# Kernel optimization log

Measured on AMD Instinct MI355X. Metric: run time of the kernel, lower is better.

The kernel has to match this reference:

```python
import jax, jax.numpy as jnp
import numpy as np

B, R, H, IN, L = 8, 128, 256, 512, 3
NH, DH = 4, H // 4  # attention heads


def _layernorm(x, g, b, eps=1e-5):
    mu = jnp.mean(x, axis=-1, keepdims=True)
    var = jnp.mean(jnp.square(x - mu), axis=-1, keepdims=True)
    return (x - mu) * jax.lax.rsqrt(var + eps) * g + b


def setup_inputs() -> dict:
    key = jax.random.key(0)
    ks = iter(jax.random.split(key, 40))
    s = 0.02
    d = {}
    d['x'] = jax.random.normal(next(ks), (B, IN), jnp.float32)
    d['We'] = jax.random.normal(next(ks), (IN, H), jnp.float32) * s
    d['be'] = jnp.zeros((H,), jnp.float32)
    # per-graph-layer params, stacked along leading L axis
    d['msg_W1'] = jax.random.normal(next(ks), (L, 2 * H, H), jnp.float32) * s
    d['msg_b1'] = jnp.zeros((L, H), jnp.float32)
    d['msg_W2'] = jax.random.normal(next(ks), (L, H, H), jnp.float32) * s
    d['msg_b2'] = jnp.zeros((L, H), jnp.float32)
    d['upd_W1'] = jax.random.normal(next(ks), (L, 2 * H, H), jnp.float32) * s
    d['upd_b1'] = jnp.zeros((L, H), jnp.float32)
    d['upd_W2'] = jax.random.normal(next(ks), (L, H, H), jnp.float32) * s
    d['upd_b2'] = jnp.zeros((L, H), jnp.float32)
    d['ln_g'] = jnp.ones((L, H), jnp.float32)
    d['ln_b'] = jnp.zeros((L, H), jnp.float32)
    d['rule_adj'] = jax.random.normal(next(ks), (R, R), jnp.float32)
    # multihead attention (4 heads)
    d['Wq'] = jax.random.normal(next(ks), (H, H), jnp.float32) * s
    d['bq'] = jnp.zeros((H,), jnp.float32)
    d['Wk'] = jax.random.normal(next(ks), (H, H), jnp.float32) * s
    d['bk'] = jnp.zeros((H,), jnp.float32)
    d['Wv'] = jax.random.normal(next(ks), (H, H), jnp.float32) * s
    d['bv'] = jnp.zeros((H,), jnp.float32)
    d['Wo'] = jax.random.normal(next(ks), (H, H), jnp.float32) * s
    d['bo'] = jnp.zeros((H,), jnp.float32)
    # readout MLP -> num_rules logits
    d['ro_W1'] = jax.random.normal(next(ks), (H, H), jnp.float32) * s
    d['ro_b1'] = jnp.zeros((H,), jnp.float32)
    d['ro_W2'] = jax.random.normal(next(ks), (H, R), jnp.float32) * s
    d['ro_b2'] = jnp.zeros((R,), jnp.float32)
    return d


def reference(x, We, be, msg_W1, msg_b1, msg_W2, msg_b2,
              upd_W1, upd_b1, upd_W2, upd_b2, ln_g, ln_b, rule_adj,
              Wq, bq, Wk, bk, Wv, bv, Wo, bo,
              ro_W1, ro_b1, ro_W2, ro_b2):
    # node encoder, broadcast to all rule-graph nodes: [B,R,H]
    h0 = x @ We + be
    h = jnp.broadcast_to(h0[:, None, :], (B, R, H))
    # rule adjacency with self-edges excluded (loop used i != j)
    A = jax.nn.sigmoid(rule_adj) * (1.0 - jnp.eye(R, dtype=rule_adj.dtype))  # [R,R]
    for l in range(L):
        # message_net(cat(h_i, h_j)) = relu(h_i@W1a + h_j@W1b + b1)@W2 + b2
        W1a, W1b = msg_W1[l][:H], msg_W1[l][H:]
        a = h @ W1a   # [B,R,H] (receiver i part)
        bb = h @ W1b  # [B,R,H] (sender j part)
        pre = jax.nn.relu(a[:, :, None, :] + bb[:, None, :, :] + msg_b1[l])  # [B,R,R,H]
        m = pre @ msg_W2[l] + msg_b2[l]  # [B,R,R,H] message from j to i
        agg = jnp.einsum('bijh,ij->bih', m, A)  # weighted sum over senders j
        # update_net(cat(h, agg))
        Wu1a, Wu1b = upd_W1[l][:H], upd_W1[l][H:]
        u = jax.nn.relu(h @ Wu1a + agg @ Wu1b + upd_b1[l]) @ upd_W2[l] + upd_b2[l]
        h = _layernorm(h + u, ln_g[l], ln_b[l])
    # multihead self-attention over nodes
    q = (h @ Wq + bq).reshape(B, R, NH, DH)
    k = (h @ Wk + bk).reshape(B, R, NH, DH)
    v = (h @ Wv + bv).reshape(B, R, NH, DH)
    logits = jnp.einsum('bqhd,bkhd->bhqk', q, k) / jnp.sqrt(jnp.float32(DH))
    attn = jax.nn.softmax(logits, axis=-1)
    pooled = jnp.einsum('bhqk,bkhd->bqhd', attn, v).reshape(B, R, H) @ Wo + bo
    g = jnp.mean(pooled, axis=1)  # [B,H]
    rule_logits = jax.nn.relu(g @ ro_W1 + ro_b1) @ ro_W2 + ro_b2
    rule_probabilities = jax.nn.softmax(rule_logits, axis=-1)  # [B,R]
    return rule_probabilities
```

## Files before the change

kernel.cpp:

```cpp
#include <hip/hip_runtime.h>
#include <math.h>

constexpr int NB  = 8;
constexpr int NR  = 128;
constexpr int HID = 256;
constexpr int NIN = 512;
constexpr int DHD = 64;
constexpr size_t SZ = (size_t)NB * NR * HID;

struct KP {
    const float *x, *We, *be, *msg_W1, *msg_b1, *msg_W2, *msg_b2;
    const float *upd_W1, *upd_b1, *upd_W2, *upd_b2, *ln_g, *ln_b, *rule_adj;
    const float *Wq, *bq, *Wk, *bk, *Wv, *bv, *Wo, *bo, *ro_W1, *ro_b1, *ro_W2, *ro_b2;
    float* out;
    float *hu0, *hu1, *hu2;
    float *bufA, *bufBB, *bufP1, *bufU1;
    float *W2u, *mb2u, *Aw, *rsum;
    float *mW1s;
    float *h0g, *c0g, *c1g;
    float *gacc;
    float *sts;
    float *scratch;
};

__device__ __forceinline__ void gemm_core(
    float (&As)[16][68], float (&Bs)[16][64], int m0, int n0,
    const float* __restrict__ A, const float* __restrict__ B,
    float (&acc)[4][4])
{
    int tid = threadIdx.x;
    int ty = tid >> 4, tx = tid & 15;
    int arow = tid >> 2, acol = (tid & 3) << 2;
    int brow = tid >> 4, bcol = (tid & 15) << 2;
    int m = m0 + arow;

    auto loadA = [&](int k0) -> float4 {
        return *(const float4*)&A[(size_t)m * HID + k0 + acol];
    };

    float4 av = loadA(0);
    float4 bv = *(const float4*)&B[(size_t)brow * HID + n0 + bcol];

    for (int k0 = 0; k0 < HID; k0 += 16) {
        As[acol + 0][arow] = av.x;
        As[acol + 1][arow] = av.y;
        As[acol + 2][arow] = av.z;
        As[acol + 3][arow] = av.w;
        *(float4*)&Bs[brow][bcol] = bv;
        __syncthreads();
        if (k0 + 16 < HID) {
            av = loadA(k0 + 16);
            bv = *(const float4*)&B[(size_t)(k0 + 16 + brow) * HID + n0 + bcol];
        }
#pragma unroll
        for (int kk = 0; kk < 16; ++kk) {
            float4 af = *(const float4*)&As[kk][ty << 2];
            float4 bf = *(const float4*)&Bs[kk][tx << 2];
            float a_[4] = {af.x, af.y, af.z, af.w};
            float b_[4] = {bf.x, bf.y, bf.z, bf.w};
#pragma unroll
            for (int i = 0; i < 4; ++i)
#pragma unroll
                for (int j = 0; j < 4; ++j) acc[i][j] += a_[i] * b_[j];
        }
        __syncthreads();
    }
}

__device__ __forceinline__ void gemv256w(
    const float* xs, const float* __restrict__ W,
    const float* __restrict__ bias, int relu, float* ys, float* red)
{
    int tid = threadIdx.x;
    int w = tid >> 6, l = tid & 63;
    float4 acc = {0.f, 0.f, 0.f, 0.f};
    const float* Wp = W + (size_t)(w * 64) * HID + l * 4;
    const float* xp = xs + w * 64;
#pragma unroll 16
    for (int kk = 0; kk < 64; ++kk) {
        float xv = xp[kk];
        float4 wv = *(const float4*)(Wp + (size_t)kk * HID);
        acc.x += xv * wv.x; acc.y += xv * wv.y;
        acc.z += xv * wv.z; acc.w += xv * wv.w;
    }
    *(float4*)&red[w * 256 + l * 4] = acc;
    __syncthreads();
    float v = red[tid] + red[256 + tid] + red[512 + tid] + red[768 + tid];
    if (bias) v += bias[tid];
    if (relu) v = fmaxf(v, 0.0f);
    ys[tid] = v;
    __syncthreads();
}

__global__ __launch_bounds__(256) void setup0_kernel(KP P) {
    __shared__ union {
        struct { float As[16][68]; float Bs[16][64]; } g;
        struct { float xs[NIN]; float part[8][32]; } e;
    } L;
    int blk = blockIdx.x;
    int t = threadIdx.x;

    if (blk < 32) {
        int rr = blk * 4 + (t >> 6);
        int l = t & 63;
        float s_loc = 0.f;
#pragma unroll
        for (int rep = 0; rep < 2; ++rep) {
            int j = l + rep * 64;
            float xv = P.rule_adj[rr * NR + j];
            float sg = 1.0f / (1.0f + expf(-xv));
            if (j == rr) sg = 0.0f;
            P.Aw[rr * NR + j] = sg;
            s_loc += sg;
        }
#pragma unroll
        for (int off = 32; off; off >>= 1) s_loc += __shfl_xor(s_loc, off);
        if (l == 0) P.rsum[rr] = s_loc;
    } else if (blk < 80) {
        int idx = blk - 32, l2 = idx >> 4, t16 = idx & 15;
        int m0 = (t16 >> 2) * 64, n0 = (t16 & 3) * 64;
        float acc[4][4] = {};
        gemm_core(L.g.As, L.g.Bs, m0, n0,
                  P.msg_W2 + (size_t)l2 * HID * HID,
                  P.upd_W1 + (size_t)l2 * 2 * HID * HID + (size_t)HID * HID,
                  acc);
        int ty = t >> 4, tx = t & 15;
        float* C = P.W2u + (size_t)l2 * HID * HID;
#pragma unroll
        for (int i = 0; i < 4; ++i) {
            int m = m0 + (ty << 2) + i, n = n0 + (tx << 2);
            float4 o = {acc[i][0], acc[i][1], acc[i][2], acc[i][3]};
            *(float4*)&C[(size_t)m * HID + n] = o;
        }
    } else if (blk < 83) {
        int l2 = blk - 80;
        const float* b2v = P.msg_b2 + l2 * HID;
        const float* Bm = P.upd_W1 + (size_t)l2 * 2 * HID * HID + (size_t)HID * HID;
        float acc = 0.f;
#pragma unroll 4
        for (int k = 0; k < HID; ++k) acc += b2v[k] * Bm[(size_t)k * HID + t];
        P.mb2u[l2 * HID + t] = acc;
    } else if (blk < 147) {
        int idx = blk - 83;
        int b = idx >> 3, s = idx & 7;
        L.e.xs[t]       = P.x[b * NIN + t];
        L.e.xs[256 + t] = P.x[b * NIN + 256 + t];
        __syncthreads();
        int c = t & 31, seg = t >> 5;
        int col = s * 32 + c;
        const float* Wp = P.We + (size_t)(seg * 64) * HID + col;
        const float* xp = L.e.xs + seg * 64;
        float acc = 0.f;
#pragma unroll 16
        for (int k = 0; k < 64; ++k) acc += xp[k] * Wp[(size_t)k * HID];
        L.e.part[seg][c] = acc;
        __syncthreads();
        if (t < 32) {
            float v = 0.f;
#pragma unroll
            for (int sg = 0; sg < 8; ++sg) v += L.e.part[sg][t];
            int cc = s * 32 + t;
            P.h0g[b * HID + cc] = v + P.be[cc];
        }
    } else if (blk < 163) {
        int base = (blk - 147) * 4096;
        for (int i = t; i < 4096; i += 256) {
            int o = base + i;
            P.mW1s[o] = P.msg_W1[o] + P.msg_W1[65536 + o];
        }
    } else {
        int pfid = blk - 163, npf = 256 - 163;
        const float* arr[11] = {P.We, P.msg_W1, P.msg_W2, P.upd_W1, P.upd_W2,
                                P.Wq, P.Wk, P.Wv, P.Wo, P.ro_W1, P.ro_W2};
        const int n4[11] = {32768, 98304, 49152, 98304, 49152,
                            16384, 16384, 16384, 16384, 16384, 8192};
        float s = 0.f;
        for (int a = 0; a < 11; ++a) {
            const float4* p4 = (const float4*)arr[a];
            for (int i = pfid * 256 + t; i < n4[a]; i += npf * 256) {
                float4 v = p4[i];
                s += v.x + v.y + v.z + v.w;
            }
        }
        if (s == 1.0e37f) P.scratch[pfid] = s;
    }
}

__global__ __launch_bounds__(256) void headc_kernel(KP P) {
    __shared__ float h0s[HID];
    __shared__ float p0s[HID];
    __shared__ float part[8][32];
    int blk = blockIdx.x;
    int z = blk >> 6, bs = blk & 63;
    int b = bs >> 3, s = bs & 7;
    int t = threadIdx.x;
    h0s[t] = P.h0g[b * HID + t];
    __syncthreads();
    const float* Wslice;
    const float* xs;
    if (z == 0) {
        Wslice = P.upd_W1;
        xs = h0s;
    } else {
        float accp = 0.f;
#pragma unroll 8
        for (int k = 0; k < HID; ++k)
            accp += h0s[k] * P.mW1s[(size_t)k * HID + t];
        p0s[t] = fmaxf(accp + P.msg_b1[t], 0.0f);
        __syncthreads();
        Wslice = P.W2u;
        xs = p0s;
    }
    int c = t & 31, seg = t >> 5;
    int col = s * 32 + c;
    const float* Wp = Wslice + (size_t)(seg * 32) * HID + col;
    const float* xp = xs + seg * 32;
    float acc = 0.f;
#pragma unroll 8
    for (int k = 0; k < 32; ++k) acc += xp[k] * Wp[(size_t)k * HID];
    part[seg][c] = acc;
    __syncthreads();
    if (t < 32) {
        float v = 0.f;
#pragma unroll
        for (int sg = 0; sg < 8; ++sg) v += part[sg][t];
        int cc = s * 32 + t;
        if (z == 0) P.c0g[b * HID + cc] = v;
        else        P.c1g[b * HID + cc] = v + P.mb2u[cc];
    }
}

__device__ __forceinline__ void rows4_matmul(
    const float (&rows)[4][HID], const float* __restrict__ W, int n, float o[4])
{
    o[0] = o[1] = o[2] = o[3] = 0.f;
#pragma unroll 4
    for (int k0 = 0; k0 < HID; k0 += 4) {
        float w0 = W[(size_t)(k0 + 0) * HID + n];
        float w1 = W[(size_t)(k0 + 1) * HID + n];
        float w2 = W[(size_t)(k0 + 2) * HID + n];
        float w3 = W[(size_t)(k0 + 3) * HID + n];
#pragma unroll
        for (int ii = 0; ii < 4; ++ii) {
            float4 rv = *(const float4*)&rows[ii][k0];
            o[ii] += rv.x * w0 + rv.y * w1 + rv.z * w2 + rv.w * w3;
        }
    }
}

__device__ __forceinline__ void row_stats4(
    float (&sred)[4][4][2], const float v[4], float* sts, float* stq, int m0)
{
    int w = threadIdx.x >> 6, l = threadIdx.x & 63;
    float s[4], q[4];
#pragma unroll
    for (int ii = 0; ii < 4; ++ii) { s[ii] = v[ii]; q[ii] = v[ii] * v[ii]; }
#pragma unroll
    for (int off = 32; off; off >>= 1) {
#pragma unroll
        for (int ii = 0; ii < 4; ++ii) {
            s[ii] += __shfl_xor(s[ii], off);
            q[ii] += __shfl_xor(q[ii], off);
        }
    }
    if (l == 0) {
#pragma unroll
        for (int ii = 0; ii < 4; ++ii) { sred[w][ii][0] = s[ii]; sred[w][ii][1] = q[ii]; }
    }
    __syncthreads();
    if (threadIdx.x < 8) {
        int row = threadIdx.x >> 1, isq = threadIdx.x & 1;
        float tot = sred[0][row][isq] + sred[1][row][isq] +
                    sred[2][row][isq] + sred[3][row][isq];
        (isq ? stq : sts)[m0 + row] = tot;
    }
}

__global__ __launch_bounds__(256) void layer0r_kernel(KP P) {
    __shared__ float u1s[4][HID];
    __shared__ float sred[4][4][2];
    int blk = blockIdx.x;
    int m0 = blk * 4;
    int b = m0 >> 7, i0 = m0 & 127;
    int t = threadIdx.x;

    float c0v = P.c0g[b * HID + t];
    float c1v = P.c1g[b * HID + t];
    float ubv = P.upd_b1[t];
#pragma unroll
    for (int ii = 0; ii < 4; ++ii)
        u1s[ii][t] = fmaxf(c0v + P.rsum[i0 + ii] * c1v + ubv, 0.0f);
    __syncthreads();

    float u[4];
    rows4_matmul(u1s, P.upd_W2, t, u);

    float h0v = P.h0g[b * HID + t] + P.upd_b2[t];
    float v[4];
#pragma unroll
    for (int ii = 0; ii < 4; ++ii) {
        v[ii] = u[ii] + h0v;
        P.hu0[(size_t)(m0 + ii) * HID + t] = v[ii];
    }
    __syncthreads();
    row_stats4(sred, v, P.sts, P.sts + 1024, m0);
}

__global__ __launch_bounds__(256) void gemm3_kernel(
    const float* __restrict__ A, const float* __restrict__ ssum, const float* __restrict__ ssq,
    const float* __restrict__ lng, const float* __restrict__ lnb,
    const float* __restrict__ B0, const float* __restrict__ B1, const float* __restrict__ B2,
    const float* __restrict__ bias0, const float* __restrict__ bias1, const float* __restrict__ bias2,
    float* __restrict__ C0, float* __restrict__ C1, float* __restrict__ C2)
{
    __shared__ float As[32][36];
    __shared__ float Bs[32][64];
    int blk = blockIdx.x;
    int z = blk >> 7, tile = blk & 127;
    const float* B    = (z == 0) ? B0 : (z == 1) ? B1 : B2;
    const float* bias = (z == 0) ? bias0 : (z == 1) ? bias1 : bias2;
    float* C          = (z == 0) ? C0 : (z == 1) ? C1 : C2;
    int m0 = (tile >> 2) * 32, n0 = (tile & 3) * 64;

    int tid = threadIdx.x;
    int ar = tid >> 3;
    int acol = (tid & 7) << 2;
    int brow = tid >> 4;
    int bcol = (tid & 15) << 2;
    int m = m0 + ar;

    bool ln = (ssum != nullptr);
    float mu = 0.f, inv = 1.f;
    if (ln) {
        float s = ssum[m], q = ssq[m];
        mu = s * (1.0f / HID);
        inv = rsqrtf(q * (1.0f / HID) - mu * mu + 1e-5f);
    }
    auto loadA = [&](int k0) -> float4 {
        int kx = k0 + acol;
        float4 v = *(const float4*)&A[(size_t)m * HID + kx];
        if (ln) {
            float4 g = *(const float4*)(lng + kx);
            float4 b = *(const float4*)(lnb + kx);
            v.x = (v.x - mu) * inv * g.x + b.x;
            v.y = (v.y - mu) * inv * g.y + b.y;
            v.z = (v.z - mu) * inv * g.z + b.z;
            v.w = (v.w - mu) * inv * g.w + b.w;
        }
        return v;
    };

    float acc[2][4] = {};
    float4 av  = loadA(0);
    float4 bv0 = *(const float4*)&B[(size_t)brow * HID + n0 + bcol];
    float4 bv1 = *(const float4*)&B[(size_t)(16 + brow) * HID + n0 + bcol];

    int ty = tid >> 4, tx = tid & 15;
    int r0 = ty << 1;

    for (int k0 = 0; k0 < HID; k0 += 32) {
        As[acol + 0][ar] = av.x;
        As[acol + 1][ar] = av.y;
        As[acol + 2][ar] = av.z;
        As[acol + 3][ar] = av.w;
        *(float4*)&Bs[brow][bcol]      = bv0;
        *(float4*)&Bs[brow + 16][bcol] = bv1;
        __syncthreads();
        if (k0 + 32 < HID) {
            av  = loadA(k0 + 32);
            bv0 = *(const float4*)&B[(size_t)(k0 + 32 + brow) * HID + n0 + bcol];
            bv1 = *(const float4*)&B[(size_t)(k0 + 48 + brow) * HID + n0 + bcol];
        }
#pragma unroll
        for (int kk = 0; kk < 32; ++kk) {
            float a0 = As[kk][r0];
            float a1 = As[kk][r0 + 1];
            float4 bf = *(const float4*)&Bs[kk][tx << 2];
            acc[0][0] += a0 * bf.x; acc[0][1] += a0 * bf.y;
            acc[0][2] += a0 * bf.z; acc[0][3] += a0 * bf.w;
            acc[1][0] += a1 * bf.x; acc[1][1] += a1 * bf.y;
            acc[1][2] += a1 * bf.z; acc[1][3] += a1 * bf.w;
        }
        __syncthreads();
    }

#pragma unroll
    for (int i = 0; i < 2; ++i) {
        int mm = m0 + r0 + i, n = n0 + (tx << 2);
        float4 o = {acc[i][0], acc[i][1], acc[i][2], acc[i][3]};
        if (bias) {
            float4 bb = *(const float4*)&bias[n];
            o.x += bb.x; o.y += bb.y; o.z += bb.z; o.w += bb.w;
        }
        *(float4*)&C[(size_t)mm * HID + n] = o;
    }
}

__global__ __launch_bounds__(256) void agg_u1r_kernel(
    const float* __restrict__ a, const float* __restrict__ bbv,
    const float* __restrict__ mb1, const float* __restrict__ Aw,
    const float* __restrict__ P1, const float* __restrict__ W2u,
    const float* __restrict__ mb2u, const float* __restrict__ rsum,
    const float* __restrict__ ub1,
    const float* __restrict__ uW2, const float* __restrict__ ub2,
    const float* __restrict__ huprev, const float* __restrict__ sP, const float* __restrict__ qP,
    const float* __restrict__ lngp, const float* __restrict__ lnbp,
    float* __restrict__ hunew, float* __restrict__ sN, float* __restrict__ qN,
    float* __restrict__ gzero)
{
    __shared__ float ap[4][HID];
    __shared__ float u1s[4][HID];
    __shared__ float sred[4][4][2];
    int blk = blockIdx.x;
    int b  = blk >> 5;
    int i0 = (blk & 31) * 4;
    int m0 = b * NR + i0;
    int t  = threadIdx.x;

    if (gzero && blk == 0) {
#pragma unroll
        for (int i = 0; i < 8; ++i) gzero[i * 256 + t] = 0.f;
    }

    float bias = mb1[t];
    float ai[4], acc[4] = {0.f, 0.f, 0.f, 0.f};
#pragma unroll
    for (int ii = 0; ii < 4; ++ii)
        ai[ii] = a[(size_t)(m0 + ii) * HID + t] + bias;
    const float* bbb = &bbv[(size_t)b * NR * HID + t];
#pragma unroll 4
    for (int j = 0; j < NR; ++j) {
        float bj = bbb[(size_t)j * HID];
#pragma unroll
        for (int ii = 0; ii < 4; ++ii) {
            float pre = fmaxf(ai[ii] + bj, 0.0f);
            acc[ii] += Aw[(i0 + ii) * NR + j] * pre;
        }
    }
#pragma unroll
    for (int ii = 0; ii < 4; ++ii) ap[ii][t] = acc[ii];
    __syncthreads();

    float w2[4];
    rows4_matmul(ap, W2u, t, w2);
    float mbv = mb2u[t], ubv = ub1[t];
#pragma unroll
    for (int ii = 0; ii < 4; ++ii) {
        float vv = w2[ii] + P1[(size_t)(m0 + ii) * HID + t] + rsum[i0 + ii] * mbv + ubv;
        u1s[ii][t] = fmaxf(vv, 0.0f);
    }
    __syncthreads();

    float u[4];
    rows4_matmul(u1s, uW2, t, u);

    float gv = lngp[t], btv = lnbp[t], ub2v = ub2[t];
    float v[4];
#pragma unroll
    for (int ii = 0; ii < 4; ++ii) {
        int m = m0 + ii;
        float sp = sP[m], qp = qP[m];
        float mup = sp * (1.0f / HID);
        float invp = rsqrtf(qp * (1.0f / HID) - mup * mup + 1e-5f);
        float hp = huprev[(size_t)m * HID + t];
        v[ii] = (hp - mup) * invp * gv + btv + u[ii] + ub2v;
        hunew[(size_t)m * HID + t] = v[ii];
    }
    __syncthreads();
    row_stats4(sred, v, sN, qN, m0);
}

__global__ __launch_bounds__(256) void attention_kernel(
    const float* __restrict__ q, const float* __restrict__ k,
    const float* __restrict__ v, float* __restrict__ gacc)
{
    __shared__ struct { float KhT[64][128]; float S[16][128]; float qs[16][64]; } L;
    int blk = blockIdx.x;
    int bh = blk >> 3, ig = blk & 7;
    int b = bh >> 2, hd = bh & 3;
    int i0 = ig * 16;
    int t = threadIdx.x;
    const float* qg = q + ((size_t)b * NR) * HID + hd * DHD;
    const float* kg = k + ((size_t)b * NR) * HID + hd * DHD;
    const float* vg = v + ((size_t)b * NR) * HID + hd * DHD;

    {
        int j = t >> 1, half = t & 1;
        const float* krow = kg + (size_t)j * HID + half * 32;
#pragma unroll
        for (int c = 0; c < 32; c += 4) {
            float4 kv = *(const float4*)(krow + c);
            L.KhT[half * 32 + c + 0][j] = kv.x;
            L.KhT[half * 32 + c + 1][j] = kv.y;
            L.KhT[half * 32 + c + 2][j] = kv.z;
            L.KhT[half * 32 + c + 3][j] = kv.w;
        }
    }
    {
        int ii = t >> 4, d0 = (t & 15) * 4;
        *(float4*)&L.qs[ii][d0] = *(const float4*)(qg + (size_t)(i0 + ii) * HID + d0);
    }
    __syncthreads();
    {
        int j = t & 127, ii2 = t >> 7;
        float acc[8] = {0.f,0.f,0.f,0.f,0.f,0.f,0.f,0.f};
#pragma unroll 4
        for (int d = 0; d < 64; ++d) {
            float kv = L.KhT[d][j];
#pragma unroll
            for (int ii = 0; ii < 8; ++ii) acc[ii] += L.qs[ii2 * 8 + ii][d] * kv;
        }
#pragma unroll
        for (int ii = 0; ii < 8; ++ii) L.S[ii2 * 8 + ii][j] = acc[ii] * 0.125f;
    }
    __syncthreads();
    {
        int w = t >> 6, l = t & 63;
#pragma unroll
        for (int r = w * 4; r < w * 4 + 4; ++r) {
            float e0 = L.S[r][l], e1 = L.S[r][l + 64];
            float mx = fmaxf(e0, e1);
#pragma unroll
            for (int off = 32; off; off >>= 1) mx = fmaxf(mx, __shfl_xor(mx, off));
            e0 = expf(e0 - mx); e1 = expf(e1 - mx);
            float sm = e0 + e1;
#pragma unroll
            for (int off = 32; off; off >>= 1) sm += __shfl_xor(sm, off);
            float inv = 1.0f / sm;
            L.S[r][l] = e0 * inv; L.S[r][l + 64] = e1 * inv;
        }
    }
    __syncthreads();
    {
        int d = t & 63, ir = t >> 6;
        float accv[4] = {0.f, 0.f, 0.f, 0.f};
        const float* vp = vg + d;
#pragma unroll 8
        for (int j = 0; j < NR; ++j) {
            float vv = vp[(size_t)j * HID];
#pragma unroll
            for (int p = 0; p < 4; ++p) accv[p] += L.S[p * 4 + ir][j] * vv;
        }
        float s = accv[0] + accv[1] + accv[2] + accv[3];
        atomicAdd(&gacc[b * HID + hd * DHD + d], s);
    }
}

__global__ __launch_bounds__(256) void tailf_kernel(KP P) {
    __shared__ float v0[HID], v1[HID], v2[HID];
    __shared__ float red[1024];
    int b = blockIdx.x;
    int t = threadIdx.x;
    int w = t >> 6, l = t & 63;

    v0[t] = P.gacc[b * HID + t] * (1.0f / NR);
    __syncthreads();
    gemv256w(v0, P.Wo, P.bo, 0, v1, red);
    gemv256w(v1, P.ro_W1, P.ro_b1, 1, v2, red);

    {
        float2 acc = {0.f, 0.f};
        const float* Wp = P.ro_W2 + (size_t)(w * 64) * NR + l * 2;
        const float* xp = v2 + w * 64;
#pragma unroll 8
        for (int kk = 0; kk < 64; ++kk) {
            float xv = xp[kk];
            float2 wv = *(const float2*)(Wp + (size_t)kk * NR);
            acc.x += xv * wv.x; acc.y += xv * wv.y;
        }
        *(float2*)&red[w * 128 + l * 2] = acc;
        __syncthreads();
    }
    float logit = -1e30f;
    if (t < NR) logit = red[t] + red[128 + t] + red[256 + t] + red[384 + t] + P.ro_b2[t];
    __syncthreads();
    float m = logit;
#pragma unroll
    for (int off = 32; off; off >>= 1) m = fmaxf(m, __shfl_xor(m, off));
    if (l == 0) red[w] = m;
    __syncthreads();
    m = fmaxf(red[0], red[1]);
    float e = (t < NR) ? expf(logit - m) : 0.0f;
    float ssum = e;
#pragma unroll
    for (int off = 32; off; off >>= 1) ssum += __shfl_xor(ssum, off);
    if (l == 0) red[4 + w] = ssum;
    __syncthreads();
    float tot = red[4] + red[5];
    if (t < NR) P.out[b * NR + t] = e / tot;
}

extern "C" void kernel_launch(void* const* d_in, const int* in_sizes, int n_in,
                              void* d_out, int out_size, void* d_ws, size_t ws_size,
                              hipStream_t stream)
{
    KP P;
    P.x        = (const float*)d_in[0];
    P.We       = (const float*)d_in[1];
    P.be       = (const float*)d_in[2];
    P.msg_W1   = (const float*)d_in[3];
    P.msg_b1   = (const float*)d_in[4];
    P.msg_W2   = (const float*)d_in[5];
    P.msg_b2   = (const float*)d_in[6];
    P.upd_W1   = (const float*)d_in[7];
    P.upd_b1   = (const float*)d_in[8];
    P.upd_W2   = (const float*)d_in[9];
    P.upd_b2   = (const float*)d_in[10];
    P.ln_g     = (const float*)d_in[11];
    P.ln_b     = (const float*)d_in[12];
    P.rule_adj = (const float*)d_in[13];
    P.Wq       = (const float*)d_in[14];
    P.bq       = (const float*)d_in[15];
    P.Wk       = (const float*)d_in[16];
    P.bk       = (const float*)d_in[17];
    P.Wv       = (const float*)d_in[18];
    P.bv       = (const float*)d_in[19];
    P.Wo       = (const float*)d_in[20];
    P.bo       = (const float*)d_in[21];
    P.ro_W1    = (const float*)d_in[22];
    P.ro_b1    = (const float*)d_in[23];
    P.ro_W2    = (const float*)d_in[24];
    P.ro_b2    = (const float*)d_in[25];
    P.out      = (float*)d_out;

    float* b0 = (float*)d_ws;
    P.hu0    = b0;  b0 += SZ;
    P.hu1    = b0;  b0 += SZ;
    P.hu2    = b0;  b0 += SZ;
    P.bufA   = b0;  b0 += SZ;
    P.bufBB  = b0;  b0 += SZ;
    P.bufP1  = b0;  b0 += SZ;
    P.bufU1  = b0;  b0 += SZ;
    P.W2u    = b0;  b0 += 3 * HID * HID;
    P.mb2u   = b0;  b0 += 3 * HID;
    P.mW1s   = b0;  b0 += HID * HID;
    P.Aw     = b0;  b0 += NR * NR;
    P.rsum   = b0;  b0 += NR;
    P.h0g    = b0;  b0 += NB * HID;
    P.c0g    = b0;  b0 += NB * HID;
    P.c1g    = b0;  b0 += NB * HID;
    P.gacc   = b0;  b0 += NB * HID;
    P.sts    = b0;  b0 += 3 * 2048;
    P.scratch= b0;  b0 += 256;

    const float* hu[3] = {P.hu0, P.hu1, P.hu2};

    setup0_kernel<<<dim3(256), 256, 0, stream>>>(P);

    headc_kernel<<<dim3(128), 256, 0, stream>>>(P);

    layer0r_kernel<<<dim3(256), 256, 0, stream>>>(P);

    for (int l = 1; l < 3; ++l) {
        const float* mW1 = P.msg_W1 + (size_t)l * 2 * HID * HID;
        const float* sP  = P.sts + (l - 1) * 2048;
        const float* qP  = sP + 1024;
        const float* lgp = P.ln_g + (size_t)(l - 1) * HID;
        const float* lbp = P.ln_b + (size_t)(l - 1) * HID;

        gemm3_kernel<<<dim3(384), 256, 0, stream>>>(
            hu[l - 1], sP, qP, lgp, lbp,
            mW1, mW1 + (size_t)HID * HID, P.upd_W1 + (size_t)l * 2 * HID * HID,
            nullptr, nullptr, nullptr,
            P.bufA, P.bufBB, P.bufP1);

        agg_u1r_kernel<<<dim3(256), 256, 0, stream>>>(
            P.bufA, P.bufBB, P.msg_b1 + (size_t)l * HID, P.Aw,
            P.bufP1, P.W2u + (size_t)l * HID * HID,
            P.mb2u + l * HID, P.rsum, P.upd_b1 + (size_t)l * HID,
            P.upd_W2 + (size_t)l * HID * HID, P.upd_b2 + (size_t)l * HID,
            hu[l - 1], sP, qP, lgp, lbp,
            (float*)hu[l], P.sts + l * 2048, P.sts + l * 2048 + 1024,
            (l == 2) ? P.gacc : nullptr);
    }

    gemm3_kernel<<<dim3(384), 256, 0, stream>>>(
        hu[2], P.sts + 2 * 2048, P.sts + 2 * 2048 + 1024,
        P.ln_g + 2 * HID, P.ln_b + 2 * HID,
        P.Wq, P.Wk, P.Wv, P.bq, P.bk, P.bv,
        P.bufA, P.bufBB, P.bufU1);

    attention_kernel<<<dim3(256), 256, 0, stream>>>(P.bufA, P.bufBB, P.bufU1, P.gacc);

    tailf_kernel<<<dim3(8), 256, 0, stream>>>(P);
}
```

Measured before the change: 274.5 us.

## Fuse layernorm and next-layer projections into aggregation kernels, drop GEMM launches

Removes the separate gemm3 launches. Each row-block kernel now computes its own full layernorm and immediately runs the next layer's three projections (msg W1a/W1b, upd W1a, or Q/K/V) on those 4 normalized rows, using per-thread rows4_matmul. Buffers are double-buffered (aB/aA) so the fused kernel can write next-layer inputs while reading the current ones. It also stages adjacency rows in shared memory. The cost is that the projections switch from tiled shared-memory GEMMs to 4-row matvecs, which re-read the weight matrices once per 4-row block and so generate more global/L2 weight traffic.

After: 293.0 us. +6.8%, slower.

```diff
diff --git a/kernel.cpp b/kernel.cpp
--- a/kernel.cpp
+++ b/kernel.cpp
@@ -13,13 +13,13 @@
     const float *upd_W1, *upd_b1, *upd_W2, *upd_b2, *ln_g, *ln_b, *rule_adj;
     const float *Wq, *bq, *Wk, *bk, *Wv, *bv, *Wo, *bo, *ro_W1, *ro_b1, *ro_W2, *ro_b2;
     float* out;
-    float *hu0, *hu1, *hu2;
-    float *bufA, *bufBB, *bufP1, *bufU1;
+    float *N0, *N1, *N2;
+    float *aB, *bbB, *p1B;
+    float *aA, *bbA, *p1A;
     float *W2u, *mb2u, *Aw, *rsum;
     float *mW1s;
     float *h0g, *c0g, *c1g;
     float *gacc;
-    float *sts;
     float *scratch;
 };
 
@@ -34,11 +34,7 @@
     int brow = tid >> 4, bcol = (tid & 15) << 2;
     int m = m0 + arow;
 
-    auto loadA = [&](int k0) -> float4 {
-        return *(const float4*)&A[(size_t)m * HID + k0 + acol];
-    };
-
-    float4 av = loadA(0);
+    float4 av = *(const float4*)&A[(size_t)m * HID + acol];
     float4 bv = *(const float4*)&B[(size_t)brow * HID + n0 + bcol];
 
     for (int k0 = 0; k0 < HID; k0 += 16) {
@@ -49,7 +45,7 @@
         *(float4*)&Bs[brow][bcol] = bv;
         __syncthreads();
         if (k0 + 16 < HID) {
-            av = loadA(k0 + 16);
+            av = *(const float4*)&A[(size_t)m * HID + k0 + 16 + acol];
             bv = *(const float4*)&B[(size_t)(k0 + 16 + brow) * HID + n0 + bcol];
         }
 #pragma unroll
@@ -89,6 +85,55 @@
     if (bias) v += bias[tid];
     if (relu) v = fmaxf(v, 0.0f);
     ys[tid] = v;
+    __syncthreads();
+}
+
+__device__ __forceinline__ void rows4_matmul(
+    const float (&rows)[4][HID], const float* __restrict__ W, int n, float o[4])
+{
+    o[0] = o[1] = o[2] = o[3] = 0.f;
+#pragma unroll 4
+    for (int k0 = 0; k0 < HID; k0 += 4) {
+        float w0 = W[(size_t)(k0 + 0) * HID + n];
+        float w1 = W[(size_t)(k0 + 1) * HID + n];
+        float w2 = W[(size_t)(k0 + 2) * HID + n];
+        float w3 = W[(size_t)(k0 + 3) * HID + n];
+#pragma unroll
+        for (int ii = 0; ii < 4; ++ii) {
+            float4 rv = *(const float4*)&rows[ii][k0];
+            o[ii] += rv.x * w0 + rv.y * w1 + rv.z * w2 + rv.w * w3;
+        }
+    }
+}
+
+__device__ __forceinline__ void ln_stats4_loc(
+    float (&sred)[4][4][2], float (&mi)[4][2], const float v[4])
+{
+    int w = threadIdx.x >> 6, l = threadIdx.x & 63;
+    float s[4], q[4];
+#pragma unroll
+    for (int ii = 0; ii < 4; ++ii) { s[ii] = v[ii]; q[ii] = v[ii] * v[ii]; }
+#pragma unroll
+    for (int off = 32; off; off >>= 1) {
+#pragma unroll
+        for (int ii = 0; ii < 4; ++ii) {
+            s[ii] += __shfl_xor(s[ii], off);
+            q[ii] += __shfl_xor(q[ii], off);
+        }
+    }
+    if (l == 0) {
+#pragma unroll
+        for (int ii = 0; ii < 4; ++ii) { sred[w][ii][0] = s[ii]; sred[w][ii][1] = q[ii]; }
+    }
+    __syncthreads();
+    if (threadIdx.x < 4) {
+        int r = threadIdx.x;
+        float ss = sred[0][r][0] + sred[1][r][0] + sred[2][r][0] + sred[3][r][0];
+        float qq = sred[0][r][1] + sred[1][r][1] + sred[2][r][1] + sred[3][r][1];
+        float mu = ss * (1.0f / HID);
+        mi[r][0] = mu;
+        mi[r][1] = rsqrtf(qq * (1.0f / HID) - mu * mu + 1e-5f);
+    }
     __syncthreads();
 }
 
@@ -230,55 +275,11 @@
     }
 }
 
-__device__ __forceinline__ void rows4_matmul(
-    const float (&rows)[4][HID], const float* __restrict__ W, int n, float o[4])
-{
-    o[0] = o[1] = o[2] = o[3] = 0.f;
-#pragma unroll 4
-    for (int k0 = 0; k0 < HID; k0 += 4) {
-        float w0 = W[(size_t)(k0 + 0) * HID + n];
-        float w1 = W[(size_t)(k0 + 1) * HID + n];
-        float w2 = W[(size_t)(k0 + 2) * HID + n];
-        float w3 = W[(size_t)(k0 + 3) * HID + n];
-#pragma unroll
-        for (int ii = 0; ii < 4; ++ii) {
-            float4 rv = *(const float4*)&rows[ii][k0];
-            o[ii] += rv.x * w0 + rv.y * w1 + rv.z * w2 + rv.w * w3;
-        }
-    }
-}
-
-__device__ __forceinline__ void row_stats4(
-    float (&sred)[4][4][2], const float v[4], float* sts, float* stq, int m0)
-{
-    int w = threadIdx.x >> 6, l = threadIdx.x & 63;
-    float s[4], q[4];
-#pragma unroll
-    for (int ii = 0; ii < 4; ++ii) { s[ii] = v[ii]; q[ii] = v[ii] * v[ii]; }
-#pragma unroll
-    for (int off = 32; off; off >>= 1) {
-#pragma unroll
-        for (int ii = 0; ii < 4; ++ii) {
-            s[ii] += __shfl_xor(s[ii], off);
-            q[ii] += __shfl_xor(q[ii], off);
-        }
-    }
-    if (l == 0) {
-#pragma unroll
-        for (int ii = 0; ii < 4; ++ii) { sred[w][ii][0] = s[ii]; sred[w][ii][1] = q[ii]; }
-    }
-    __syncthreads();
-    if (threadIdx.x < 8) {
-        int row = threadIdx.x >> 1, isq = threadIdx.x & 1;
-        float tot = sred[0][row][isq] + sred[1][row][isq] +
-                    sred[2][row][isq] + sred[3][row][isq];
-        (isq ? stq : sts)[m0 + row] = tot;
-    }
-}
-
-__global__ __launch_bounds__(256) void layer0r_kernel(KP P) {
+__global__ __launch_bounds__(256) void layer0p_kernel(KP P) {
     __shared__ float u1s[4][HID];
+    __shared__ float nrm[4][HID];
     __shared__ float sred[4][4][2];
+    __shared__ float mi[4][2];
     int blk = blockIdx.x;
     int m0 = blk * 4;
     int b = m0 >> 7, i0 = m0 & 127;
@@ -298,119 +299,52 @@
     float h0v = P.h0g[b * HID + t] + P.upd_b2[t];
     float v[4];
 #pragma unroll
+    for (int ii = 0; ii < 4; ++ii) v[ii] = u[ii] + h0v;
+
+    ln_stats4_loc(sred, mi, v);
+    float gv = P.ln_g[t], btv = P.ln_b[t];
+#pragma unroll
     for (int ii = 0; ii < 4; ++ii) {
-        v[ii] = u[ii] + h0v;
-        P.hu0[(size_t)(m0 + ii) * HID + t] = v[ii];
-    }
-    __syncthreads();
-    row_stats4(sred, v, P.sts, P.sts + 1024, m0);
-}
-
-__global__ __launch_bounds__(256) void gemm3_kernel(
-    const float* __restrict__ A, const float* __restrict__ ssum, const float* __restrict__ ssq,
-    const float* __restrict__ lng, const float* __restrict__ lnb,
-    const float* __restrict__ B0, const float* __restrict__ B1, const float* __restrict__ B2,
-    const float* __restrict__ bias0, const float* __restrict__ bias1, const float* __restrict__ bias2,
-    float* __restrict__ C0, float* __restrict__ C1, float* __restrict__ C2)
-{
-    __shared__ float As[32][36];
-    __shared__ float Bs[32][64];
-    int blk = blockIdx.x;
-    int z = blk >> 7, tile = blk & 127;
-    const float* B    = (z == 0) ? B0 : (z == 1) ? B1 : B2;
-    const float* bias = (z == 0) ? bias0 : (z == 1) ? bias1 : bias2;
-    float* C          = (z == 0) ? C0 : (z == 1) ? C1 : C2;
-    int m0 = (tile >> 2) * 32, n0 = (tile & 3) * 64;
-
-    int tid = threadIdx.x;
-    int ar = tid >> 3;
-    int acol = (tid & 7) << 2;
-    int brow = tid >> 4;
-    int bcol = (tid & 15) << 2;
-    int m = m0 + ar;
-
-    bool ln = (ssum != nullptr);
-    float mu = 0.f, inv = 1.f;
-    if (ln) {
-        float s = ssum[m], q = ssq[m];
-        mu = s * (1.0f / HID);
-        inv = rsqrtf(q * (1.0f / HID) - mu * mu + 1e-5f);
-    }
-    auto loadA = [&](int k0) -> float4 {
-        int kx = k0 + acol;
-        float4 v = *(const float4*)&A[(size_t)m * HID + kx];
-        if (ln) {
-            float4 g = *(const float4*)(lng + kx);
-            float4 b = *(const float4*)(lnb + kx);
-            v.x = (v.x - mu) * inv * g.x + b.x;
-            v.y = (v.y - mu) * inv * g.y + b.y;
-            v.z = (v.z - mu) * inv * g.z + b.z;
-            v.w = (v.w - mu) * inv * g.w + b.w;
-        }
-        return v;
-    };
-
-    float acc[2][4] = {};
-    float4 av  = loadA(0);
-    float4 bv0 = *(const float4*)&B[(size_t)brow * HID + n0 + bcol];
-    float4 bv1 = *(const float4*)&B[(size_t)(16 + brow) * HID + n0 + bcol];
-
-    int ty = tid >> 4, tx = tid & 15;
-    int r0 = ty << 1;
-
-    for (int k0 = 0; k0 < HID; k0 += 32) {
-        As[acol + 0][ar] = av.x;
-        As[acol + 1][ar] = av.y;
-        As[acol + 2][ar] = av.z;
-        As[acol + 3][ar] = av.w;
-        *(float4*)&Bs[brow][bcol]      = bv0;
-        *(float4*)&Bs[brow + 16][bcol] = bv1;
-        __syncthreads();
-        if (k0 + 32 < HID) {
-            av  = loadA(k0 + 32);
-            bv0 = *(const float4*)&B[(size_t)(k0 + 32 + brow) * HID + n0 + bcol];
-            bv1 = *(const float4*)&B[(size_t)(k0 + 48 + brow) * HID + n0 + bcol];
-        }
-#pragma unroll
-        for (int kk = 0; kk < 32; ++kk) {
-            float a0 = As[kk][r0];
-            float a1 = As[kk][r0 + 1];
-            float4 bf = *(const float4*)&Bs[kk][tx << 2];
-            acc[0][0] += a0 * bf.x; acc[0][1] += a0 * bf.y;
-            acc[0][2] += a0 * bf.z; acc[0][3] += a0 * bf.w;
-            acc[1][0] += a1 * bf.x; acc[1][1] += a1 * bf.y;
-            acc[1][2] += a1 * bf.z; acc[1][3] += a1 * bf.w;
-        }
-        __syncthreads();
-    }
-
-#pragma unroll
-    for (int i = 0; i < 2; ++i) {
-        int mm = m0 + r0 + i, n = n0 + (tx << 2);
-        float4 o = {acc[i][0], acc[i][1], acc[i][2], acc[i][3]};
-        if (bias) {
-            float4 bb = *(const float4*)&bias[n];
-            o.x += bb.x; o.y += bb.y; o.z += bb.z; o.w += bb.w;
-        }
-        *(float4*)&C[(size_t)mm * HID + n] = o;
-    }
-}
-
-__global__ __launch_bounds__(256) void agg_u1r_kernel(
+        float nv = (v[ii] - mi[ii][0]) * mi[ii][1] * gv + btv;
+        nrm[ii][t] = nv;
+        P.N0[(size_t)(m0 + ii) * HID + t] = nv;
+    }
+    __syncthreads();
+
+    const float* mW1a1 = P.msg_W1 + (size_t)1 * 2 * HID * HID;
+    const float* uW1a1 = P.upd_W1 + (size_t)1 * 2 * HID * HID;
+    float o[4];
+    rows4_matmul(nrm, mW1a1, t, o);
+#pragma unroll
+    for (int ii = 0; ii < 4; ++ii) P.aB[(size_t)(m0 + ii) * HID + t] = o[ii];
+    rows4_matmul(nrm, mW1a1 + (size_t)HID * HID, t, o);
+#pragma unroll
+    for (int ii = 0; ii < 4; ++ii) P.bbB[(size_t)(m0 + ii) * HID + t] = o[ii];
+    rows4_matmul(nrm, uW1a1, t, o);
+#pragma unroll
+    for (int ii = 0; ii < 4; ++ii) P.p1B[(size_t)(m0 + ii) * HID + t] = o[ii];
+}
+
+__global__ __launch_bounds__(256) void aggproj_kernel(
     const float* __restrict__ a, const float* __restrict__ bbv,
     const float* __restrict__ mb1, const float* __restrict__ Aw,
+    const float* __restrict__ rsumv,
     const float* __restrict__ P1, const float* __restrict__ W2u,
-    const float* __restrict__ mb2u, const float* __restrict__ rsum,
-    const float* __restrict__ ub1,
+    const float* __restrict__ mb2u, const float* __restrict__ ub1,
     const float* __restrict__ uW2, const float* __restrict__ ub2,
-    const float* __restrict__ huprev, const float* __restrict__ sP, const float* __restrict__ qP,
-    const float* __restrict__ lngp, const float* __restrict__ lnbp,
-    float* __restrict__ hunew, float* __restrict__ sN, float* __restrict__ qN,
+    const float* __restrict__ Nprev, const float* __restrict__ lng,
+    const float* __restrict__ lnb, float* __restrict__ Nout,
+    const float* __restrict__ pw0, const float* __restrict__ pb0, float* __restrict__ o0,
+    const float* __restrict__ pw1, const float* __restrict__ pb1, float* __restrict__ o1,
+    const float* __restrict__ pw2, const float* __restrict__ pb2, float* __restrict__ o2,
     float* __restrict__ gzero)
 {
     __shared__ float ap[4][HID];
     __shared__ float u1s[4][HID];
+    __shared__ float nrm[4][HID];
+    __shared__ float awr[4][NR];
     __shared__ float sred[4][4][2];
+    __shared__ float mi[4][2];
     int blk = blockIdx.x;
     int b  = blk >> 5;
     int i0 = (blk & 31) * 4;
@@ -422,11 +356,18 @@
         for (int i = 0; i < 8; ++i) gzero[i * 256 + t] = 0.f;
     }
 
+    if (t < NR) {
+#pragma unroll
+        for (int ii = 0; ii < 4; ++ii) awr[ii][t] = Aw[(i0 + ii) * NR + t];
+    }
     float bias = mb1[t];
-    float ai[4], acc[4] = {0.f, 0.f, 0.f, 0.f};
+    float ai[4];
 #pragma unroll
     for (int ii = 0; ii < 4; ++ii)
         ai[ii] = a[(size_t)(m0 + ii) * HID + t] + bias;
+    __syncthreads();
+
+    float acc[4] = {0.f, 0.f, 0.f, 0.f};
     const float* bbb = &bbv[(size_t)b * NR * HID + t];
 #pragma unroll 4
     for (int j = 0; j < NR; ++j) {
@@ -434,7 +375,7 @@
 #pragma unroll
         for (int ii = 0; ii < 4; ++ii) {
             float pre = fmaxf(ai[ii] + bj, 0.0f);
-            acc[ii] += Aw[(i0 + ii) * NR + j] * pre;
+            acc[ii] += awr[ii][j] * pre;
         }
     }
 #pragma unroll
@@ -446,28 +387,42 @@
     float mbv = mb2u[t], ubv = ub1[t];
 #pragma unroll
     for (int ii = 0; ii < 4; ++ii) {
-        float vv = w2[ii] + P1[(size_t)(m0 + ii) * HID + t] + rsum[i0 + ii] * mbv + ubv;
+        float vv = w2[ii] + P1[(size_t)(m0 + ii) * HID + t] + rsumv[i0 + ii] * mbv + ubv;
         u1s[ii][t] = fmaxf(vv, 0.0f);
     }
     __syncthreads();
 
     float u[4];
     rows4_matmul(u1s, uW2, t, u);
-
-    float gv = lngp[t], btv = lnbp[t], ub2v = ub2[t];
+    float ub2v = ub2[t];
     float v[4];
 #pragma unroll
+    for (int ii = 0; ii < 4; ++ii)
+        v[ii] = Nprev[(size_t)(m0 + ii) * HID + t] + u[ii] + ub2v;
+
+    ln_stats4_loc(sred, mi, v);
+    float gv = lng[t], btv = lnb[t];
+#pragma unroll
     for (int ii = 0; ii < 4; ++ii) {
-        int m = m0 + ii;
-        float sp = sP[m], qp = qP[m];
-        float mup = sp * (1.0f / HID);
-        float invp = rsqrtf(qp * (1.0f / HID) - mup * mup + 1e-5f);
-        float hp = huprev[(size_t)m * HID + t];
-        v[ii] = (hp - mup) * invp * gv + btv + u[ii] + ub2v;
-        hunew[(size_t)m * HID + t] = v[ii];
-    }
-    __syncthreads();
-    row_stats4(sred, v, sN, qN, m0);
+        float nv = (v[ii] - mi[ii][0]) * mi[ii][1] * gv + btv;
+        nrm[ii][t] = nv;
+        Nout[(size_t)(m0 + ii) * HID + t] = nv;
+    }
+    __syncthreads();
+
+    float o[4];
+    rows4_matmul(nrm, pw0, t, o);
+    float p0v = pb0 ? pb0[t] : 0.f;
+#pragma unroll
+    for (int ii = 0; ii < 4; ++ii) o0[(size_t)(m0 + ii) * HID + t] = o[ii] + p0v;
+    rows4_matmul(nrm, pw1, t, o);
+    float p1v = pb1 ? pb1[t] : 0.f;
+#pragma unroll
+    for (int ii = 0; ii < 4; ++ii) o1[(size_t)(m0 + ii) * HID + t] = o[ii] + p1v;
+    rows4_matmul(nrm, pw2, t, o);
+    float p2v = pb2 ? pb2[t] : 0.f;
+#pragma unroll
+    for (int ii = 0; ii < 4; ++ii) o2[(size_t)(m0 + ii) * HID + t] = o[ii] + p2v;
 }
 
 __global__ __launch_bounds__(256) void attention_kernel(
@@ -624,13 +579,15 @@
     P.out      = (float*)d_out;
 
     float* b0 = (float*)d_ws;
-    P.hu0    = b0;  b0 += SZ;
-    P.hu1    = b0;  b0 += SZ;
-    P.hu2    = b0;  b0 += SZ;
-    P.bufA   = b0;  b0 += SZ;
-    P.bufBB  = b0;  b0 += SZ;
-    P.bufP1  = b0;  b0 += SZ;
-    P.bufU1  = b0;  b0 += SZ;
+    P.N0     = b0;  b0 += SZ;
+    P.N1     = b0;  b0 += SZ;
+    P.N2     = b0;  b0 += SZ;
+    P.aB     = b0;  b0 += SZ;
+    P.bbB    = b0;  b0 += SZ;
+    P.p1B    = b0;  b0 += SZ;
+    P.aA     = b0;  b0 += SZ;
+    P.bbA    = b0;  b0 += SZ;
+    P.p1A    = b0;  b0 += SZ;
     P.W2u    = b0;  b0 += 3 * HID * HID;
     P.mb2u   = b0;  b0 += 3 * HID;
     P.mW1s   = b0;  b0 += HID * HID;
@@ -640,47 +597,45 @@
     P.c0g    = b0;  b0 += NB * HID;
     P.c1g    = b0;  b0 += NB * HID;
     P.gacc   = b0;  b0 += NB * HID;
-    P.sts    = b0;  b0 += 3 * 2048;
     P.scratch= b0;  b0 += 256;
 
-    const float* hu[3] = {P.hu0, P.hu1, P.hu2};
-
     setup0_kernel<<<dim3(256), 256, 0, stream>>>(P);
 
     headc_kernel<<<dim3(128), 256, 0, stream>>>(P);
 
-    layer0r_kernel<<<dim3(256), 256, 0, stream>>>(P);
-
-    for (int l = 1; l < 3; ++l) {
-        const float* mW1 = P.msg_W1 + (size_t)l * 2 * HID * HID;
-        const float* sP  = P.sts + (l - 1) * 2048;
-        const float* qP  = sP + 1024;
-        const float* lgp = P.ln_g + (size_t)(l - 1) * HID;
-        const float* lbp = P.ln_b + (size_t)(l - 1) * HID;
-
-        gemm3_kernel<<<dim3(384), 256, 0, stream>>>(
-            hu[l - 1], sP, qP, lgp, lbp,
-            mW1, mW1 + (size_t)HID * HID, P.upd_W1 + (size_t)l * 2 * HID * HID,
-            nullptr, nullptr, nullptr,
-            P.bufA, P.bufBB, P.bufP1);
-
-        agg_u1r_kernel<<<dim3(256), 256, 0, stream>>>(
-            P.bufA, P.bufBB, P.msg_b1 + (size_t)l * HID, P.Aw,
-            P.bufP1, P.W2u + (size_t)l * HID * HID,
-            P.mb2u + l * HID, P.rsum, P.upd_b1 + (size_t)l * HID,
+    layer0p_kernel<<<dim3(256), 256, 0, stream>>>(P);
+
+    {
+        const int l = 1;
+        const float* mW1a2 = P.msg_W1 + (size_t)2 * 2 * HID * HID;
+        const float* uW1a2 = P.upd_W1 + (size_t)2 * 2 * HID * HID;
+        aggproj_kernel<<<dim3(256), 256, 0, stream>>>(
+            P.aB, P.bbB, P.msg_b1 + (size_t)l * HID, P.Aw, P.rsum,
+            P.p1B, P.W2u + (size_t)l * HID * HID, P.mb2u + l * HID,
+            P.upd_b1 + (size_t)l * HID,
             P.upd_W2 + (size_t)l * HID * HID, P.upd_b2 + (size_t)l * HID,
-            hu[l - 1], sP, qP, lgp, lbp,
-            (float*)hu[l], P.sts + l * 2048, P.sts + l * 2048 + 1024,
-            (l == 2) ? P.gacc : nullptr);
-    }
-
-    gemm3_kernel<<<dim3(384), 256, 0, stream>>>(
-        hu[2], P.sts + 2 * 2048, P.sts + 2 * 2048 + 1024,
-        P.ln_g + 2 * HID, P.ln_b + 2 * HID,
-        P.Wq, P.Wk, P.Wv, P.bq, P.bk, P.bv,
-        P.bufA, P.bufBB, P.bufU1);
-
-    attention_kernel<<<dim3(256), 256, 0, stream>>>(P.bufA, P.bufBB, P.bufU1, P.gacc);
+            P.N0, P.ln_g + (size_t)l * HID, P.ln_b + (size_t)l * HID, P.N1,
+            mW1a2, nullptr, P.aA,
+            mW1a2 + (size_t)HID * HID, nullptr, P.bbA,
+            uW1a2, nullptr, P.p1A,
+            nullptr);
+    }
+
+    {
+        const int l = 2;
+        aggproj_kernel<<<dim3(256), 256, 0, stream>>>(
+            P.aA, P.bbA, P.msg_b1 + (size_t)l * HID, P.Aw, P.rsum,
+            P.p1A, P.W2u + (size_t)l * HID * HID, P.mb2u + l * HID,
+            P.upd_b1 + (size_t)l * HID,
+            P.upd_W2 + (size_t)l * HID * HID, P.upd_b2 + (size_t)l * HID,
+            P.N1, P.ln_g + (size_t)l * HID, P.ln_b + (size_t)l * HID, P.N2,
+            P.Wq, P.bq, P.aB,
+            P.Wk, P.bk, P.bbB,
+            P.Wv, P.bv, P.p1B,
+            P.gacc);
+    }
+
+    attention_kernel<<<dim3(256), 256, 0, stream>>>(P.aB, P.bbB, P.p1B, P.gacc);
 
     tailf_kernel<<<dim3(8), 256, 0, stream>>>(P);
 }
```
